# Kernel tuning notes

Measured on AMD Instinct MI355X. Metric: run time of the kernel, lower is better.

The kernel has to match this reference:

```python
import jax, jax.numpy as jnp
import numpy as np

N, M, K, C = 2048, 2048, 32, 256
AW, NE, H, S = 32, 128, 8, 32
LMAX = 2
HID = min(128, AW // 2)          # 16, hidden width of radial MLPs
EC = AW + NE + C                 # 416, edge feature dim
M0 = 2 * AW * (LMAX + 1)         # 192, q/k degree-dot feature dim
SLICES = [(0, 1), (1, 4), (4, 9)]  # m-slices for l = 0, 1, 2


def _ln(x, g, b, eps=1e-5):
    mu = jnp.mean(x, -1, keepdims=True)
    var = jnp.mean(jnp.square(x - mu), -1, keepdims=True)
    return (x - mu) * jax.lax.rsqrt(var + eps) * g + b


def _radial(x, w1, b1, g1, be1, w2, b2, g2, be2, w3, b3):
    # EquiformerV2-style RadialFunction: Linear->LN->SiLU x2 -> Linear
    h = jax.nn.silu(_ln(x @ w1.T + b1, g1, be1))
    h = jax.nn.silu(_ln(h @ w2.T + b2, g2, be2))
    return h @ w3.T + b3


def _so3_linear(x, W, b):
    # per-degree channel mixing; bias only on l=0. x: [..., 9, Cin], W: [3, Cout, Cin]
    outs = []
    for l, (s, e) in enumerate(SLICES):
        o = jnp.einsum('...mc,dc->...md', x[..., s:e, :], W[l])
        if l == 0:
            o = o + b
        outs.append(o)
    return jnp.concatenate(outs, axis=-2)


def _sph_all(vec):
    # real spherical harmonics l=0..2 of normalized vec, integral normalization
    v = vec / (jnp.linalg.norm(vec, axis=-1, keepdims=True) + 1e-12)
    x, y, z = v[..., 0], v[..., 1], v[..., 2]
    y0 = jnp.full(x.shape, 0.28209479177387814)
    c1 = 0.4886025119029199
    c2a, c2b, c2c = 1.0925484305920792, 0.31539156525252005, 0.5462742152960396
    return jnp.stack([y0, c1 * y, c1 * z, c1 * x,
                      c2a * x * y, c2a * y * z, c2b * (3.0 * z * z - 1.0),
                      c2a * x * z, c2c * (x * x - y * y)], axis=-1)


def _smooth_leaky(x, a=0.2):
    return 0.5 * (1 + a) * x + 0.5 * (1 - a) * x * (2.0 * jax.nn.sigmoid(x) - 1.0)


def _forward(node_pos, node_irreps_input, edge_dis, edge_vec, attn_weight,
             cluster_irreps_input, tgt_emb, W_dot, b_dot,
             rm0_w1, rm0_b1, rm0_g1, rm0_be1, rm0_w2, rm0_b2, rm0_g2, rm0_be2, rm0_w3, rm0_b3,
             fc_m0_w, fc_m0_b, an_g, an_b, alpha_dot,
             rv_w1, rv_b1, rv_g1, rv_be1, rv_w2, rv_b2, rv_g2, rv_be2, rv_w3, rv_b3,
             wz, bz, atomic_numbers, attn_mask, f_sparse_idx_expnode):
    n, k = attn_weight.shape[0], attn_weight.shape[1]
    aw = jnp.where(attn_mask, 0.0, attn_weight)                 # mask padded neighbors
    tgt = tgt_emb[atomic_numbers]                               # [N,NE]
    idx = f_sparse_idx_expnode                                  # [N,K] cluster gather index
    cl_scal = cluster_irreps_input[:, 0, :][idx]                # [N,K,C] scalar (l=0) part
    x_edge = jnp.concatenate(
        [aw, jnp.broadcast_to(tgt[:, None, :], (n, k, tgt.shape[-1])), cl_scal], -1)

    # dot_alpha attention logits: per-degree <feat, Y_l(r_ij)> for query and gathered key
    q = _so3_linear(node_irreps_input, W_dot, b_dot)            # [N,9,AW]
    key = _so3_linear(cluster_irreps_input, W_dot, b_dot)[idx]  # [N,K,9,AW]
    sh = _sph_all(edge_vec)                                     # [N,K,9]
    dots = [jnp.einsum('nmc,nkm->nkc', q[:, s:e, :], sh[..., s:e]) for s, e in SLICES]
    dots += [jnp.einsum('nkmc,nkm->nkc', key[:, :, s:e, :], sh[..., s:e]) for s, e in SLICES]
    m0 = jnp.concatenate(dots, -1)                              # [N,K,M0]

    ew = _radial(x_edge, rm0_w1, rm0_b1, rm0_g1, rm0_be1, rm0_w2, rm0_b2, rm0_g2, rm0_be2, rm0_w3, rm0_b3)
    af = ((m0 * ew) @ fc_m0_w.T + fc_m0_b).reshape(n, k, H, S)
    af = _smooth_leaky(_ln(af, an_g, an_b))
    logits = jnp.einsum('nkhs,hs->nkh', af, alpha_dot)
    logits = jnp.where(attn_mask, -1e9, logits)
    alpha = jax.nn.softmax(logits, axis=1)                      # [N,K,H]

    # zero-order value path: radial edge weight modulates gathered equivariant values
    vw = _radial(x_edge, rv_w1, rv_b1, rv_g1, rv_be1, rv_w2, rv_b2, rv_g2, rv_be2, rv_w3, rv_b3)
    v = (cluster_irreps_input[idx] * vw[:, :, None, :]).reshape(n, k, 9, H, C // H)
    out = jnp.einsum('nkh,nkmhc->nmhc', alpha, v).reshape(n, 9, C)
    return _so3_linear(out, wz, bz)                             # [N,9,C]


def setup_inputs() -> dict:
    ks = iter(jax.random.split(jax.random.key(0), 64))
    nrm = lambda shape, s=1.0: jax.random.normal(next(ks), shape, jnp.float32) * s
    inp = {}
    inp['node_pos'] = nrm((N, 3))
    inp['node_irreps_input'] = nrm((N, 9, C))
    inp['edge_dis'] = jax.random.uniform(next(ks), (N, K), jnp.float32) * 5.0
    inp['edge_vec'] = nrm((N, K, 3))
    inp['attn_weight'] = nrm((N, K, AW))
    inp['atomic_numbers'] = jax.random.randint(next(ks), (N,), 0, 256)
    inp['attn_mask'] = jax.random.bernoulli(next(ks), 0.1, (N, K, 1))
    inp['f_sparse_idx_expnode'] = jax.random.randint(next(ks), (N, K), 0, M)
    inp['cluster_irreps_input'] = nrm((M, 9, C))
    inp['tgt_emb'] = jax.random.uniform(next(ks), (256, NE), jnp.float32, -0.001, 0.001)
    inp['W_dot'] = nrm((3, AW, C), C ** -0.5)
    inp['b_dot'] = jnp.zeros((AW,), jnp.float32)

    def rad_params(pfx, out_dim):
        d = {}
        d[pfx + '_w1'] = nrm((HID, EC), EC ** -0.5); d[pfx + '_b1'] = jnp.zeros((HID,), jnp.float32)
        d[pfx + '_g1'] = jnp.ones((HID,), jnp.float32); d[pfx + '_be1'] = jnp.zeros((HID,), jnp.float32)
        d[pfx + '_w2'] = nrm((HID, HID), HID ** -0.5); d[pfx + '_b2'] = jnp.zeros((HID,), jnp.float32)
        d[pfx + '_g2'] = jnp.ones((HID,), jnp.float32); d[pfx + '_be2'] = jnp.zeros((HID,), jnp.float32)
        d[pfx + '_w3'] = nrm((out_dim, HID), HID ** -0.5); d[pfx + '_b3'] = jnp.zeros((out_dim,), jnp.float32)
        return d

    inp.update(rad_params('rm0', M0))
    inp['fc_m0_w'] = nrm((H * S, M0), M0 ** -0.5)
    inp['fc_m0_b'] = jnp.zeros((H * S,), jnp.float32)
    inp['an_g'] = jnp.ones((S,), jnp.float32)
    inp['an_b'] = jnp.zeros((S,), jnp.float32)
    std = S ** -0.5
    inp['alpha_dot'] = jax.random.uniform(next(ks), (H, S), jnp.float32, -std, std)
    inp.update(rad_params('rv', C))
    inp['wz'] = nrm((3, C, C), C ** -0.5)
    inp['bz'] = jnp.zeros((C,), jnp.float32)
    return inp


def reference(node_pos, node_irreps_input, edge_dis, edge_vec, attn_weight, atomic_numbers,
              attn_mask, f_sparse_idx_expnode, cluster_irreps_input, tgt_emb, W_dot, b_dot,
              rm0_w1, rm0_b1, rm0_g1, rm0_be1, rm0_w2, rm0_b2, rm0_g2, rm0_be2, rm0_w3, rm0_b3,
              fc_m0_w, fc_m0_b, an_g, an_b, alpha_dot,
              rv_w1, rv_b1, rv_g1, rv_be1, rv_w2, rv_b2, rv_g2, rv_be2, rv_w3, rv_b3,
              wz, bz):
    return _forward(node_pos, node_irreps_input, edge_dis, edge_vec, attn_weight,
                    cluster_irreps_input, tgt_emb, W_dot, b_dot,
                    rm0_w1, rm0_b1, rm0_g1, rm0_be1, rm0_w2, rm0_b2, rm0_g2, rm0_be2, rm0_w3, rm0_b3,
                    fc_m0_w, fc_m0_b, an_g, an_b, alpha_dot,
                    rv_w1, rv_b1, rv_g1, rv_be1, rv_w2, rv_b2, rv_g2, rv_be2, rv_w3, rv_b3,
                    wz, bz, atomic_numbers, attn_mask, f_sparse_idx_expnode)
```

## Files before the change

### kernel.cpp

```cpp
#include <hip/hip_runtime.h>
#include <math.h>

#define NNODE 2048
#define MCLUS 2048
#define KNBR  32
#define CDIM  256
#define HHEAD 8

typedef __attribute__((ext_vector_type(8))) short bf16x8;
typedef __attribute__((ext_vector_type(4))) float f32x4;

__device__ __forceinline__ float sigf(float x) { return 1.0f / (1.0f + __expf(-x)); }

__device__ __forceinline__ unsigned short f2bf(float f) {
    unsigned x = __float_as_uint(f);
    unsigned r = ((x >> 16) & 1u) + 0x7FFFu;
    return (unsigned short)((x + r) >> 16);
}
__device__ __forceinline__ float bf2f(unsigned short u) {
    return __uint_as_float(((unsigned)u) << 16);
}

__device__ __forceinline__ bool edge_masked(const void* mp, int mode, int e) {
    if (mode & 2) return ((const float*)mp)[e] != 0.0f;
    if (mode & 1) return ((const unsigned char*)mp)[e] != 0;
    return ((const int*)mp)[e] != 0;
}

__global__ __launch_bounds__(256) void kprep(
    const unsigned int* __restrict__ mw, int* __restrict__ flag,
    const float* __restrict__ clus, const float* __restrict__ fcw,
    const float* __restrict__ wz,
    unsigned short* __restrict__ clh, unsigned short* __restrict__ fcwh,
    unsigned short* __restrict__ wzh,
    const float* __restrict__ tgt_emb,
    const float* __restrict__ rm0_w1, const float* __restrict__ rv_w1,
    float* __restrict__ TA, float* __restrict__ CA,
    const float* __restrict__ nodei, const float* __restrict__ W_dot,
    const float* __restrict__ b_dot,
    float* __restrict__ q_ws, unsigned short* __restrict__ keyh)
{
    __shared__ __align__(16) unsigned short Xb[32][264];
    __shared__ __align__(16) unsigned short Wb[32][264];
    __shared__ int rx[32], rmm[32];
    int b = blockIdx.x, t = threadIdx.x;

    if (b < 1152) {
        int l, vr0, nm, moff;
        if (b < 128)      { l = 0; vr0 = b * 32;         nm = 1; moff = 0; }
        else if (b < 512) { l = 1; vr0 = (b - 128) * 32; nm = 3; moff = 1; }
        else              { l = 2; vr0 = (b - 512) * 32; nm = 5; moff = 4; }
        if (t < 32) {
            int vr = vr0 + t;
            rx[t] = vr / nm;
            rmm[t] = moff + vr % nm;
        }
        __syncthreads();
        for (int e = t; e < 32 * 256; e += 256) {
            int r = e >> 8, c = e & 255;
            int x = rx[r], m = rmm[r];
            const float* src = (x < NNODE) ? (nodei + ((size_t)x * 9 + m) * 256)
                                           : (clus + ((size_t)(x - NNODE) * 9 + m) * 256);
            Xb[r][c] = f2bf(src[c]);
            Wb[r][c] = f2bf(W_dot[((size_t)l * 32 + r) * 256 + c]);
        }
        __syncthreads();

        int wid = t >> 6, lane = t & 63;
        int lrow = lane & 15, kgrp = lane >> 4;
        int mt = wid >> 1, nt = wid & 1;
        f32x4 acc = (f32x4){0.f, 0.f, 0.f, 0.f};
#pragma unroll
        for (int kk = 0; kk < 8; ++kk) {
            bf16x8 a8 = *(const bf16x8*)&Xb[mt * 16 + lrow][kk * 32 + kgrp * 8];
            bf16x8 b8 = *(const bf16x8*)&Wb[nt * 16 + lrow][kk * 32 + kgrp * 8];
            acc = __builtin_amdgcn_mfma_f32_16x16x32_bf16(a8, b8, acc, 0, 0, 0);
        }
        int dcol = nt * 16 + lrow;
        float bias = (l == 0) ? b_dot[dcol] : 0.0f;
#pragma unroll
        for (int r = 0; r < 4; ++r) {
            int row = mt * 16 + kgrp * 4 + r;
            int x = rx[row], m = rmm[row];
            float val = acc[r] + bias;
            if (x < NNODE) q_ws[((size_t)x * 9 + m) * 32 + dcol] = val;
            else           keyh[((size_t)(x - NNODE) * 9 + m) * 32 + dcol] = f2bf(val);
        }
    } else if (b < 4160) {
        int bb = b - 1152;
        if (bb < MCLUS) {
            size_t base = (size_t)bb * 2304;
#pragma unroll
            for (int r = 0; r < 9; ++r) {
                int o = r * 256 + t;
                clh[base + o] = f2bf(clus[base + o]);
            }
        } else if (bb < MCLUS + 192) {
            int off = (bb - MCLUS) * 256 + t;
            fcwh[off] = f2bf(fcw[off]);
        } else {
            int off = (bb - MCLUS - 192) * 256 + t;
            wzh[off] = f2bf(wz[off]);
        }
    } else if (b < 4448) {
        int bb = b - 4160;
        int slot = t & 31, j = slot & 15, mlp = slot >> 4;
        const float* w1 = mlp ? rv_w1 : rm0_w1;
        if (bb < 32) {
            int a = bb * 8 + (t >> 5);
            const float* x = tgt_emb + (size_t)a * 128;
            const float* w = w1 + j * 416 + 32;
            float acc = 0.0f;
            for (int i = 0; i < 128; i += 4)
                acc = fmaf(x[i], w[i], fmaf(x[i+1], w[i+1], fmaf(x[i+2], w[i+2], fmaf(x[i+3], w[i+3], acc))));
            TA[a * 32 + slot] = acc;
        } else {
            int m = (bb - 32) * 8 + (t >> 5);
            const float* x = clus + (size_t)m * 2304;
            const float* w = w1 + j * 416 + 160;
            float acc = 0.0f;
            for (int i = 0; i < 256; i += 4)
                acc = fmaf(x[i], w[i], fmaf(x[i+1], w[i+1], fmaf(x[i+2], w[i+2], fmaf(x[i+3], w[i+3], acc))));
            CA[m * 32 + slot] = acc;
        }
    } else {
        int i = (b - 4448) * 256 + t;
        unsigned int w = mw[i];
        int vb = (w != 0u && w != 1u && w != 0x3F800000u) ? 1 : 0;
        int vf = (w == 0x3F800000u) ? 1 : 0;
        unsigned long long bal_b = __ballot(vb);
        unsigned long long bal_f = __ballot(vf);
        if ((t & 63) == 0) {
            if (bal_b) atomicOr(flag, 1);
            if (bal_f) atomicOr(flag, 2);
        }
    }
}

__device__ __forceinline__ float lnsilu16(float x, float g, float b) {
    float s = x;
#pragma unroll
    for (int m = 1; m < 16; m <<= 1) s += __shfl_xor(s, m, 16);
    float mu = s * 0.0625f;
    float d = x - mu;
    float s2 = d * d;
#pragma unroll
    for (int m = 1; m < 16; m <<= 1) s2 += __shfl_xor(s2, m, 16);
    float y = d * rsqrtf(s2 * 0.0625f + 1e-5f) * g + b;
    return y * sigf(y);
}

__global__ __launch_bounds__(256, 2) void k2abc(
    const float* __restrict__ attn_weight, const void* __restrict__ mask,
    const int* __restrict__ mflag,
    const int* __restrict__ f_idx, const float* __restrict__ edge_vec,
    const int* __restrict__ atom_num, const unsigned short* __restrict__ clh,
    const float* __restrict__ q_ws, const unsigned short* __restrict__ keyh,
    const float* __restrict__ TA, const float* __restrict__ CA,
    const float* __restrict__ rm0_w1, const float* __restrict__ rm0_b1,
    const float* __restrict__ rm0_g1, const float* __restrict__ rm0_be1,
    const float* __restrict__ rm0_w2, const float* __restrict__ rm0_b2,
    const float* __restrict__ rm0_g2, const float* __restrict__ rm0_be2,
    const float* __restrict__ rm0_w3, const float* __restrict__ rm0_b3,
    const unsigned short* __restrict__ fcwh, const float* __restrict__ fcb,
    const float* __restrict__ an_g, const float* __restrict__ an_b,
    const float* __restrict__ alpha_dot,
    const float* __restrict__ rv_w1, const float* __restrict__ rv_b1,
    const float* __restrict__ rv_g1, const float* __restrict__ rv_be1,
    const float* __restrict__ rv_w2, const float* __restrict__ rv_b2,
    const float* __restrict__ rv_g2, const float* __restrict__ rv_be2,
    const float* __restrict__ rv_w3, const float* __restrict__ rv_b3,
    float* __restrict__ outpre)
{
    __shared__ float qn[288];
    __shared__ float Ts[32];
    __shared__ float shS[32][9];
    __shared__ __align__(16) unsigned char poolS[32 * 200 * 2];
    float (*awS)[32] = (float(*)[32])poolS;
    float (*caS)[32] = (float(*)[32])(poolS + 4096);
    unsigned short (*mwbS)[200] = (unsigned short(*)[200])poolS;
    __shared__ __align__(16) unsigned char pool2[6144];
    unsigned short (*KDSh)[96] = (unsigned short(*)[96])pool2;
    float (*lgS)[8] = (float(*)[8])pool2;
    float* alS = (float*)(pool2 + 1024);
    float* mxS = (float*)(pool2 + 2048);
    float* invS = (float*)(pool2 + 2080);
    __shared__ float h2mS[32][17];
    __shared__ float h2vS[32][17];
    __shared__ int idxk[32], maskk[32];

    int n = blockIdx.x, t = threadIdx.x;
    int mode = mflag[0];

    for (int i = t; i < 288; i += 256) qn[i] = q_ws[(size_t)n * 288 + i];
    if (t < 32) {
        int an = atom_num[n];
        Ts[t] = TA[an * 32 + t];
        int e = n * KNBR + t;
        idxk[t] = f_idx[e];
        maskk[t] = edge_masked(mask, mode, e) ? 1 : 0;
        float vx = edge_vec[(size_t)e * 3 + 0];
        float vy = edge_vec[(size_t)e * 3 + 1];
        float vz = edge_vec[(size_t)e * 3 + 2];
        float inv = 1.0f / (sqrtf(vx * vx + vy * vy + vz * vz) + 1e-12f);
        float x = vx * inv, y = vy * inv, z = vz * inv;
        shS[t][0] = 0.28209479177387814f;
        shS[t][1] = 0.4886025119029199f * y;
        shS[t][2] = 0.4886025119029199f * z;
        shS[t][3] = 0.4886025119029199f * x;
        shS[t][4] = 1.0925484305920792f * x * y;
        shS[t][5] = 1.0925484305920792f * y * z;
        shS[t][6] = 0.31539156525252005f * (3.0f * z * z - 1.0f);
        shS[t][7] = 1.0925484305920792f * x * z;
        shS[t][8] = 0.5462742152960396f * (x * x - y * y);
    }
    __syncthreads();
    for (int e2 = t; e2 < 1024; e2 += 256) {
        int ek = e2 >> 5, i = e2 & 31;
        awS[ek][i] = maskk[ek] ? 0.0f : attn_weight[((size_t)(n * KNBR + ek)) * 32 + i];
        caS[ek][i] = CA[(size_t)idxk[ek] * 32 + i];
    }
    for (int i = t; i < 32 * 96; i += 256) {
        int e = i / 96, j = i - e * 96;
        int p = j >> 5, c = j & 31;
        const unsigned short* kr = keyh + (size_t)idxk[e] * 288;
        float v;
        if (p == 0)      v = bf2f(kr[c]) * shS[e][0];
        else if (p == 1) v = bf2f(kr[32 + c]) * shS[e][1] + bf2f(kr[64 + c]) * shS[e][2]
                           + bf2f(kr[96 + c]) * shS[e][3];
        else             v = bf2f(kr[128 + c]) * shS[e][4] + bf2f(kr[160 + c]) * shS[e][5]
                           + bf2f(kr[192 + c]) * shS[e][6] + bf2f(kr[224 + c]) * shS[e][7]
                           + bf2f(kr[256 + c]) * shS[e][8];
        KDSh[e][j] = f2bf(v);
    }
    __syncthreads();

    {
        int g = t >> 4, j = t & 15;
        for (int ee = 0; ee < 2; ++ee) {
            int e = g + ee * 16;
            float accm = rm0_b1[j] + Ts[j] + caS[e][j];
            float accv = rv_b1[j] + Ts[16 + j] + caS[e][16 + j];
            const float* w1m = rm0_w1 + j * 416;
            const float* w1v = rv_w1 + j * 416;
#pragma unroll
            for (int i = 0; i < 32; i += 4) {
                float a0 = awS[e][i], a1 = awS[e][i + 1], a2 = awS[e][i + 2], a3 = awS[e][i + 3];
                accm = fmaf(a0, w1m[i], fmaf(a1, w1m[i+1], fmaf(a2, w1m[i+2], fmaf(a3, w1m[i+3], accm))));
                accv = fmaf(a0, w1v[i], fmaf(a1, w1v[i+1], fmaf(a2, w1v[i+2], fmaf(a3, w1v[i+3], accv))));
            }
            float hm = lnsilu16(accm, rm0_g1[j], rm0_be1[j]);
            float hv = lnsilu16(accv, rv_g1[j], rv_be1[j]);
            float am2 = rm0_b2[j], av2 = rv_b2[j];
#pragma unroll
            for (int i = 0; i < 16; ++i) {
                am2 = fmaf(__shfl(hm, i, 16), rm0_w2[j * 16 + i], am2);
                av2 = fmaf(__shfl(hv, i, 16), rv_w2[j * 16 + i], av2);
            }
            float h2m = lnsilu16(am2, rm0_g2[j], rm0_be2[j]);
            float h2v = lnsilu16(av2, rv_g2[j], rv_be2[j]);
            h2vS[e][j] = h2v;
            h2mS[e][j] = h2m;
        }
    }
    __syncthreads();

#pragma unroll
    for (int bb = 0; bb < 6; ++bb) {
#pragma unroll
        for (int r2 = 0; r2 < 4; ++r2) {
            int oi = r2 * 256 + t;
            int e = oi >> 5, c = oi & 31;
            int d = bb * 32 + c;
            const float4* w3 = (const float4*)(rm0_w3 + d * 16);
            float ew = rm0_b3[d];
#pragma unroll
            for (int i4 = 0; i4 < 4; ++i4) {
                float4 w = w3[i4];
                ew = fmaf(h2mS[e][i4 * 4 + 0], w.x, fmaf(h2mS[e][i4 * 4 + 1], w.y,
                     fmaf(h2mS[e][i4 * 4 + 2], w.z, fmaf(h2mS[e][i4 * 4 + 3], w.w, ew))));
            }
            float m0v;
            if (bb == 0)      m0v = qn[c] * shS[e][0];
            else if (bb == 1) m0v = qn[32 + c] * shS[e][1] + qn[64 + c] * shS[e][2]
                                  + qn[96 + c] * shS[e][3];
            else if (bb == 2) m0v = qn[128 + c] * shS[e][4] + qn[160 + c] * shS[e][5]
                                  + qn[192 + c] * shS[e][6] + qn[224 + c] * shS[e][7]
                                  + qn[256 + c] * shS[e][8];
            else              m0v = bf2f(KDSh[e][(bb - 3) * 32 + c]);
            mwbS[e][d] = f2bf(ew * m0v);
        }
    }
    __syncthreads();

    {
        int wid = t >> 6, lane = t & 63;
        int lrow = lane & 15, kgrp = lane >> 4;
        f32x4 acc[4][2];
#pragma unroll
        for (int i = 0; i < 4; ++i)
#pragma unroll
            for (int m = 0; m < 2; ++m) acc[i][m] = (f32x4){0.f, 0.f, 0.f, 0.f};

#pragma unroll
        for (int ntl = 0; ntl < 4; ++ntl) {
            int col = wid * 64 + ntl * 16 + lrow;
            const bf16x8* brow = (const bf16x8*)(fcwh + (size_t)col * 192);
            bf16x8 bf[6];
#pragma unroll
            for (int kk = 0; kk < 6; ++kk) bf[kk] = brow[kk * 4 + kgrp];
#pragma unroll
            for (int kk = 0; kk < 6; ++kk) {
#pragma unroll
                for (int m = 0; m < 2; ++m) {
                    bf16x8 a8 = *(const bf16x8*)&mwbS[m * 16 + lrow][kk * 32 + kgrp * 8];
                    acc[ntl][m] = __builtin_amdgcn_mfma_f32_16x16x32_bf16(a8, bf[kk], acc[ntl][m], 0, 0, 0);
                }
            }
        }
#pragma unroll
        for (int ntl = 0; ntl < 4; ++ntl) {
            float fb = fcb[wid * 64 + ntl * 16 + lrow];
#pragma unroll
            for (int m = 0; m < 2; ++m)
#pragma unroll
                for (int r = 0; r < 4; ++r) acc[ntl][m][r] += fb;
        }
        float ang0 = an_g[lrow], ang1 = an_g[16 + lrow];
        float anb0 = an_b[lrow], anb1 = an_b[16 + lrow];
#pragma unroll
        for (int hh = 0; hh < 2; ++hh) {
            int h = wid * 2 + hh;
            float ad0 = alpha_dot[h * 32 + lrow], ad1 = alpha_dot[h * 32 + 16 + lrow];
#pragma unroll
            for (int m = 0; m < 2; ++m) {
#pragma unroll
                for (int r = 0; r < 4; ++r) {
                    float a = acc[2 * hh][m][r], b = acc[2 * hh + 1][m][r];
                    float su = a + b;
#pragma unroll
                    for (int mm = 1; mm < 16; mm <<= 1) su += __shfl_xor(su, mm, 16);
                    float mu = su * (1.0f / 32.0f);
                    float da = a - mu, db = b - mu;
                    float v2 = da * da + db * db;
#pragma unroll
                    for (int mm = 1; mm < 16; mm <<= 1) v2 += __shfl_xor(v2, mm, 16);
                    float rs = rsqrtf(v2 * (1.0f / 32.0f) + 1e-5f);
                    float y0 = da * rs * ang0 + anb0;
                    float y1 = db * rs * ang1 + anb1;
                    float sl0 = 0.6f * y0 + 0.4f * y0 * (2.0f * sigf(y0) - 1.0f);
                    float sl1 = 0.6f * y1 + 0.4f * y1 * (2.0f * sigf(y1) - 1.0f);
                    float lg = sl0 * ad0 + sl1 * ad1;
#pragma unroll
                    for (int mm = 1; mm < 16; mm <<= 1) lg += __shfl_xor(lg, mm, 16);
                    if (lrow == 0) {
                        int e = m * 16 + kgrp * 4 + r;
                        lgS[e][h] = maskk[e] ? -1e9f : lg;
                    }
                }
            }
        }
    }
    __syncthreads();

    if (t < 8) {
        float mx = -1e30f;
#pragma unroll
        for (int k = 0; k < 32; ++k) mx = fmaxf(mx, lgS[k][t]);
        float sum = 0.0f;
#pragma unroll
        for (int k = 0; k < 32; ++k) sum += __expf(lgS[k][t] - mx);
        mxS[t] = mx;
        invS[t] = 1.0f / sum;
    }
    __syncthreads();
    {
        int k = t >> 3, h = t & 7;
        alS[t] = __expf(lgS[k][h] - mxS[h]) * invS[h];
    }
    __syncthreads();

    {
        int c = t, h = c >> 5;
        float w3r[16];
        const float4* w3p = (const float4*)(rv_w3 + c * 16);
#pragma unroll
        for (int i4 = 0; i4 < 4; ++i4) {
            float4 w = w3p[i4];
            w3r[i4 * 4 + 0] = w.x; w3r[i4 * 4 + 1] = w.y;
            w3r[i4 * 4 + 2] = w.z; w3r[i4 * 4 + 3] = w.w;
        }
        float b3c = rv_b3[c];
        float acc[9];
#pragma unroll
        for (int m = 0; m < 9; ++m) acc[m] = 0.0f;
        for (int k = 0; k < 32; ++k) {
            if (maskk[k]) continue;
            float vw = b3c;
#pragma unroll
            for (int i = 0; i < 16; ++i) vw = fmaf(h2vS[k][i], w3r[i], vw);
            float av = alS[k * 8 + h] * vw;
            const unsigned short* crow = clh + (size_t)idxk[k] * 2304 + c;
#pragma unroll
            for (int m = 0; m < 9; ++m) acc[m] = fmaf(av, bf2f(crow[m * 256]), acc[m]);
        }
#pragma unroll
        for (int m = 0; m < 9; ++m) outpre[((size_t)n * 9 + m) * 256 + c] = acc[m];
    }
}

__global__ __launch_bounds__(256) void k5_final(
    const unsigned short* __restrict__ wzh, const float* __restrict__ bz,
    float* __restrict__ io)
{
    __shared__ __align__(16) unsigned short Xb[32][264];
    __shared__ int rr[32];
    int b = blockIdx.x, t = threadIdx.x;
    int l, vr0, nm, moff;
    if (b < 64)       { l = 0; vr0 = b * 32;         nm = 1; moff = 0; }
    else if (b < 256) { l = 1; vr0 = (b - 64) * 32;  nm = 3; moff = 1; }
    else              { l = 2; vr0 = (b - 256) * 32; nm = 5; moff = 4; }
    if (t < 32) {
        int vr = vr0 + t;
        int n = vr / nm, m = moff + vr % nm;
        rr[t] = n * 9 + m;
    }
    __syncthreads();
    for (int e = t; e < 32 * 256; e += 256) {
        int r = e >> 8, c = e & 255;
        Xb[r][c] = f2bf(io[(size_t)rr[r] * 256 + c]);
    }
    __syncthreads();

    int wid = t >> 6, lane = t & 63;
    int lrow = lane & 15, kgrp = lane >> 4;
    f32x4 acc[2][4];
#pragma unroll
    for (int mt = 0; mt < 2; ++mt)
#pragma unroll
        for (int ntl = 0; ntl < 4; ++ntl) acc[mt][ntl] = (f32x4){0.f, 0.f, 0.f, 0.f};

#pragma unroll
    for (int ntl = 0; ntl < 4; ++ntl) {
        int dcol = wid * 64 + ntl * 16 + lrow;
        const bf16x8* brow = (const bf16x8*)(wzh + ((size_t)l * 256 + dcol) * 256);
#pragma unroll
        for (int kk = 0; kk < 8; ++kk) {
            bf16x8 b8 = brow[kk * 4 + kgrp];
#pragma unroll
            for (int mt = 0; mt < 2; ++mt) {
                bf16x8 a8 = *(const bf16x8*)&Xb[mt * 16 + lrow][kk * 32 + kgrp * 8];
                acc[mt][ntl] = __builtin_amdgcn_mfma_f32_16x16x32_bf16(a8, b8, acc[mt][ntl], 0, 0, 0);
            }
        }
    }
#pragma unroll
    for (int ntl = 0; ntl < 4; ++ntl) {
        int dcol = wid * 64 + ntl * 16 + lrow;
        float bias = (l == 0) ? bz[dcol] : 0.0f;
#pragma unroll
        for (int mt = 0; mt < 2; ++mt) {
#pragma unroll
            for (int r = 0; r < 4; ++r) {
                int row = mt * 16 + kgrp * 4 + r;
                io[(size_t)rr[row] * 256 + dcol] = acc[mt][ntl][r] + bias;
            }
        }
    }
}

extern "C" void kernel_launch(void* const* d_in, const int* in_sizes, int n_in,
                              void* d_out, int out_size, void* d_ws, size_t ws_size,
                              hipStream_t stream)
{
    (void)in_sizes; (void)n_in; (void)out_size; (void)ws_size;

    const float* node_irreps = (const float*)d_in[1];
    const float* edge_vec    = (const float*)d_in[3];
    const float* attn_weight = (const float*)d_in[4];
    const int*   atom_num    = (const int*)d_in[5];
    const void*  attn_mask   = d_in[6];
    const int*   f_idx       = (const int*)d_in[7];
    const float* clus        = (const float*)d_in[8];
    const float* tgt_emb     = (const float*)d_in[9];
    const float* W_dot       = (const float*)d_in[10];
    const float* b_dot       = (const float*)d_in[11];
    const float* rm0_w1 = (const float*)d_in[12];
    const float* rm0_b1 = (const float*)d_in[13];
    const float* rm0_g1 = (const float*)d_in[14];
    const float* rm0_be1 = (const float*)d_in[15];
    const float* rm0_w2 = (const float*)d_in[16];
    const float* rm0_b2 = (const float*)d_in[17];
    const float* rm0_g2 = (const float*)d_in[18];
    const float* rm0_be2 = (const float*)d_in[19];
    const float* rm0_w3 = (const float*)d_in[20];
    const float* rm0_b3 = (const float*)d_in[21];
    const float* fcw = (const float*)d_in[22];
    const float* fcb = (const float*)d_in[23];
    const float* an_g = (const float*)d_in[24];
    const float* an_b = (const float*)d_in[25];
    const float* alpha_dot = (const float*)d_in[26];
    const float* rv_w1 = (const float*)d_in[27];
    const float* rv_b1 = (const float*)d_in[28];
    const float* rv_g1 = (const float*)d_in[29];
    const float* rv_be1 = (const float*)d_in[30];
    const float* rv_w2 = (const float*)d_in[31];
    const float* rv_b2 = (const float*)d_in[32];
    const float* rv_g2 = (const float*)d_in[33];
    const float* rv_be2 = (const float*)d_in[34];
    const float* rv_w3 = (const float*)d_in[35];
    const float* rv_b3 = (const float*)d_in[36];
    const float* wz = (const float*)d_in[37];
    const float* bz = (const float*)d_in[38];

    float* ws = (float*)d_ws;
    int* flag = (int*)d_ws;
    float* q_ws = ws + 16;
    unsigned short* keyh = (unsigned short*)(q_ws + (size_t)NNODE * 288);
    float* TA_ws = (float*)(keyh + (size_t)MCLUS * 288);
    float* CA_ws = TA_ws + 256 * 32;
    unsigned short* clh = (unsigned short*)(CA_ws + (size_t)MCLUS * 32);
    unsigned short* fcwh = (unsigned short*)(clh + (size_t)MCLUS * 2304);
    unsigned short* wzh = fcwh + 256 * 192;
    float* outpre = (float*)d_out;

    hipMemsetAsync(flag, 0, sizeof(int), stream);
    kprep<<<4512, 256, 0, stream>>>(
        (const unsigned int*)attn_mask, flag,
        clus, fcw, wz, clh, fcwh, wzh,
        tgt_emb, rm0_w1, rv_w1, TA_ws, CA_ws,
        node_irreps, W_dot, b_dot, q_ws, keyh);
    k2abc<<<NNODE, 256, 0, stream>>>(
        attn_weight, attn_mask, flag, f_idx, edge_vec, atom_num, clh,
        q_ws, keyh, TA_ws, CA_ws,
        rm0_w1, rm0_b1, rm0_g1, rm0_be1, rm0_w2, rm0_b2, rm0_g2, rm0_be2, rm0_w3, rm0_b3,
        fcwh, fcb, an_g, an_b, alpha_dot,
        rv_w1, rv_b1, rv_g1, rv_be1, rv_w2, rv_b2, rv_g2, rv_be2, rv_w3, rv_b3,
        outpre);
    k5_final<<<576, 256, 0, stream>>>(wzh, bz, outpre);
}
```

Before: 200.2 us.

## Halve shared memory by staging attn weights in bf16 and splitting MFMA edges

```diff
diff --git a/kernel.cpp b/kernel.cpp
--- a/kernel.cpp
+++ b/kernel.cpp
@@ -175,9 +175,9 @@
     __shared__ float qn[288];
     __shared__ float Ts[32];
     __shared__ float shS[32][9];
-    __shared__ __align__(16) unsigned char poolS[32 * 200 * 2];
-    float (*awS)[32] = (float(*)[32])poolS;
-    float (*caS)[32] = (float(*)[32])(poolS + 4096);
+    __shared__ __align__(16) unsigned char poolS[6400];
+    unsigned short (*awSh)[32] = (unsigned short(*)[32])poolS;
+    float (*caS)[32] = (float(*)[32])(poolS + 2048);
     unsigned short (*mwbS)[200] = (unsigned short(*)[200])poolS;
     __shared__ __align__(16) unsigned char pool2[6144];
     unsigned short (*KDSh)[96] = (unsigned short(*)[96])pool2;
@@ -217,7 +217,8 @@
     __syncthreads();
     for (int e2 = t; e2 < 1024; e2 += 256) {
         int ek = e2 >> 5, i = e2 & 31;
-        awS[ek][i] = maskk[ek] ? 0.0f : attn_weight[((size_t)(n * KNBR + ek)) * 32 + i];
+        awSh[ek][i] = f2bf(maskk[ek] ? 0.0f
+                          : attn_weight[((size_t)(n * KNBR + ek)) * 32 + i]);
         caS[ek][i] = CA[(size_t)idxk[ek] * 32 + i];
     }
     for (int i = t; i < 32 * 96; i += 256) {
@@ -245,7 +246,8 @@
             const float* w1v = rv_w1 + j * 416;
 #pragma unroll
             for (int i = 0; i < 32; i += 4) {
-                float a0 = awS[e][i], a1 = awS[e][i + 1], a2 = awS[e][i + 2], a3 = awS[e][i + 3];
+                float a0 = bf2f(awSh[e][i]), a1 = bf2f(awSh[e][i + 1]);
+                float a2 = bf2f(awSh[e][i + 2]), a3 = bf2f(awSh[e][i + 3]);
                 accm = fmaf(a0, w1m[i], fmaf(a1, w1m[i+1], fmaf(a2, w1m[i+2], fmaf(a3, w1m[i+3], accm))));
                 accv = fmaf(a0, w1v[i], fmaf(a1, w1v[i+1], fmaf(a2, w1v[i+2], fmaf(a3, w1v[i+3], accv))));
             }
@@ -265,59 +267,58 @@
     }
     __syncthreads();
 
-#pragma unroll
-    for (int bb = 0; bb < 6; ++bb) {
-#pragma unroll
-        for (int r2 = 0; r2 < 4; ++r2) {
-            int oi = r2 * 256 + t;
-            int e = oi >> 5, c = oi & 31;
-            int d = bb * 32 + c;
-            const float4* w3 = (const float4*)(rm0_w3 + d * 16);
-            float ew = rm0_b3[d];
-#pragma unroll
-            for (int i4 = 0; i4 < 4; ++i4) {
-                float4 w = w3[i4];
-                ew = fmaf(h2mS[e][i4 * 4 + 0], w.x, fmaf(h2mS[e][i4 * 4 + 1], w.y,
-                     fmaf(h2mS[e][i4 * 4 + 2], w.z, fmaf(h2mS[e][i4 * 4 + 3], w.w, ew))));
-            }
-            float m0v;
-            if (bb == 0)      m0v = qn[c] * shS[e][0];
-            else if (bb == 1) m0v = qn[32 + c] * shS[e][1] + qn[64 + c] * shS[e][2]
-                                  + qn[96 + c] * shS[e][3];
-            else if (bb == 2) m0v = qn[128 + c] * shS[e][4] + qn[160 + c] * shS[e][5]
-                                  + qn[192 + c] * shS[e][6] + qn[224 + c] * shS[e][7]
-                                  + qn[256 + c] * shS[e][8];
-            else              m0v = bf2f(KDSh[e][(bb - 3) * 32 + c]);
-            mwbS[e][d] = f2bf(ew * m0v);
-        }
-    }
-    __syncthreads();
-
-    {
-        int wid = t >> 6, lane = t & 63;
-        int lrow = lane & 15, kgrp = lane >> 4;
-        f32x4 acc[4][2];
-#pragma unroll
-        for (int i = 0; i < 4; ++i)
-#pragma unroll
-            for (int m = 0; m < 2; ++m) acc[i][m] = (f32x4){0.f, 0.f, 0.f, 0.f};
-
+    int wid = t >> 6, lane = t & 63;
+    int lrow = lane & 15, kgrp = lane >> 4;
+    f32x4 acc[4][2];
+#pragma unroll
+    for (int i = 0; i < 4; ++i)
+#pragma unroll
+        for (int m = 0; m < 2; ++m) acc[i][m] = (f32x4){0.f, 0.f, 0.f, 0.f};
+
+    for (int half = 0; half < 2; ++half) {
+#pragma unroll
+        for (int bb = 0; bb < 6; ++bb) {
+#pragma unroll
+            for (int r2 = 0; r2 < 2; ++r2) {
+                int oi = r2 * 256 + t;
+                int el = oi >> 5, c = oi & 31;
+                int e = half * 16 + el;
+                int d = bb * 32 + c;
+                const float4* w3 = (const float4*)(rm0_w3 + d * 16);
+                float ew = rm0_b3[d];
+#pragma unroll
+                for (int i4 = 0; i4 < 4; ++i4) {
+                    float4 w = w3[i4];
+                    ew = fmaf(h2mS[e][i4 * 4 + 0], w.x, fmaf(h2mS[e][i4 * 4 + 1], w.y,
+                         fmaf(h2mS[e][i4 * 4 + 2], w.z, fmaf(h2mS[e][i4 * 4 + 3], w.w, ew))));
+                }
+                float m0v;
+                if (bb == 0)      m0v = qn[c] * shS[e][0];
+                else if (bb == 1) m0v = qn[32 + c] * shS[e][1] + qn[64 + c] * shS[e][2]
+                                      + qn[96 + c] * shS[e][3];
+                else if (bb == 2) m0v = qn[128 + c] * shS[e][4] + qn[160 + c] * shS[e][5]
+                                      + qn[192 + c] * shS[e][6] + qn[224 + c] * shS[e][7]
+                                      + qn[256 + c] * shS[e][8];
+                else              m0v = bf2f(KDSh[e][(bb - 3) * 32 + c]);
+                mwbS[el][d] = f2bf(ew * m0v);
+            }
+        }
+        __syncthreads();
 #pragma unroll
         for (int ntl = 0; ntl < 4; ++ntl) {
             int col = wid * 64 + ntl * 16 + lrow;
             const bf16x8* brow = (const bf16x8*)(fcwh + (size_t)col * 192);
-            bf16x8 bf[6];
-#pragma unroll
-            for (int kk = 0; kk < 6; ++kk) bf[kk] = brow[kk * 4 + kgrp];
 #pragma unroll
             for (int kk = 0; kk < 6; ++kk) {
-#pragma unroll
-                for (int m = 0; m < 2; ++m) {
-                    bf16x8 a8 = *(const bf16x8*)&mwbS[m * 16 + lrow][kk * 32 + kgrp * 8];
-                    acc[ntl][m] = __builtin_amdgcn_mfma_f32_16x16x32_bf16(a8, bf[kk], acc[ntl][m], 0, 0, 0);
-                }
-            }
-        }
+                bf16x8 a8 = *(const bf16x8*)&mwbS[lrow][kk * 32 + kgrp * 8];
+                acc[ntl][half] = __builtin_amdgcn_mfma_f32_16x16x32_bf16(
+                    a8, brow[kk * 4 + kgrp], acc[ntl][half], 0, 0, 0);
+            }
+        }
+        __syncthreads();
+    }
+
+    {
 #pragma unroll
         for (int ntl = 0; ntl < 4; ++ntl) {
             float fb = fcb[wid * 64 + ntl * 16 + lrow];
@@ -391,9 +392,9 @@
             w3r[i4 * 4 + 2] = w.z; w3r[i4 * 4 + 3] = w.w;
         }
         float b3c = rv_b3[c];
-        float acc[9];
-#pragma unroll
-        for (int m = 0; m < 9; ++m) acc[m] = 0.0f;
+        float acc9[9];
+#pragma unroll
+        for (int m = 0; m < 9; ++m) acc9[m] = 0.0f;
         for (int k = 0; k < 32; ++k) {
             if (maskk[k]) continue;
             float vw = b3c;
@@ -402,10 +403,10 @@
             float av = alS[k * 8 + h] * vw;
             const unsigned short* crow = clh + (size_t)idxk[k] * 2304 + c;
 #pragma unroll
-            for (int m = 0; m < 9; ++m) acc[m] = fmaf(av, bf2f(crow[m * 256]), acc[m]);
-        }
-#pragma unroll
-        for (int m = 0; m < 9; ++m) outpre[((size_t)n * 9 + m) * 256 + c] = acc[m];
+            for (int m = 0; m < 9; ++m) acc9[m] = fmaf(av, bf2f(crow[m * 256]), acc9[m]);
+        }
+#pragma unroll
+        for (int m = 0; m < 9; ++m) outpre[((size_t)n * 9 + m) * 256 + c] = acc9[m];
     }
 }
 
```

Result: slower. 328.2 us (+63.9%).
